# Kernel optimization log

Measured on AMD Instinct MI355X. Metric: run time of the kernel, lower is better.

## Reference

```python
import jax, jax.numpy as jnp
import numpy as np

B, C, H, W = 8, 256, 64, 64
CK = 64  # C // k with k=4


def setup_inputs() -> dict:
    key = jax.random.key(0)
    ks = jax.random.split(key, 5)
    s = 1.0 / np.sqrt(C)
    return {
        "x": jax.random.normal(ks[0], (B, C, H, W), dtype=jnp.float32),
        "wq": jax.random.normal(ks[1], (CK, C), dtype=jnp.float32) * s,
        "bq": jnp.zeros((CK,), dtype=jnp.float32),
        "wk": jax.random.normal(ks[2], (CK, C), dtype=jnp.float32) * s,
        "bk": jnp.zeros((CK,), dtype=jnp.float32),
        "wv": jax.random.normal(ks[3], (C, C), dtype=jnp.float32) * s,
        "bv": jnp.zeros((C,), dtype=jnp.float32),
        "wg": jax.random.normal(ks[4], (C, C), dtype=jnp.float32) * s,
        "bg": jnp.zeros((C,), dtype=jnp.float32),
    }


def reference(x, wq, bq, wk, bk, wv, bv, wg, bg):
    b, c, h, w = x.shape
    n = h * w
    xf = x.reshape(b, c, n)  # [B, C, N]
    # 1x1 convs are channel-wise matmuls
    q = jnp.einsum('oc,bcn->bon', wq, xf) + bq[None, :, None]  # [B, Ck, N]
    k = jnp.einsum('oc,bcn->bon', wk, xf) + bk[None, :, None]  # [B, Ck, N]
    v = jnp.einsum('oc,bcn->bon', wv, xf) + bv[None, :, None]  # [B, C, N]
    # energy[b,i,j] = q[b,:,i] . k[b,:,j]
    energy = jnp.einsum('bci,bcj->bij', q, k)  # [B, N, N]
    energy = jax.nn.elu(energy) / n
    out = jnp.einsum('bcn,bnj->bcj', v, energy).reshape(b, c, h, w)
    out = jnp.einsum('oc,bchw->bohw', wg, out) + bg[None, :, None, None]
    return out
```

## Files before the change

kernel.cpp:

```cpp
#include <hip/hip_runtime.h>
#include <math.h>

#define BATCH 8
#define CH    256
#define NPIX  4096
#define CKDIM 64

typedef __attribute__((ext_vector_type(8))) short short8;
typedef __attribute__((ext_vector_type(4))) float f32x4;

#define MFMA16x16(a, b, c) __builtin_amdgcn_mfma_f32_16x16x32_bf16((a), (b), (c), 0, 0, 0)

__device__ __forceinline__ unsigned short f2bf(float f) {
    union { float f; unsigned int u; } v; v.f = f;
    unsigned int u = v.u;
    u += 0x7fffu + ((u >> 16) & 1u);
    return (unsigned short)(u >> 16);
}

__global__ void prep_kernel(const float* __restrict__ wq, const float* __restrict__ bq,
                            const float* __restrict__ wk, const float* __restrict__ bk,
                            const float* __restrict__ wv, const float* __restrict__ bv,
                            const float* __restrict__ wg,
                            unsigned short* __restrict__ W_frag, float* __restrict__ bias_all) {
    int o = blockIdx.x;
    int c = threadIdx.x;

    float val;
    if (o < 64) {
        val = wq[o * CH + c];
        if (c == 0) bias_all[o] = bq[o];
    } else if (o < 128) {
        int oo = o - 64;
        val = wk[oo * CH + c];
        if (c == 0) bias_all[o] = bk[oo];
    } else {
        __shared__ float wgr[CH];
        int oo = o - 128;
        wgr[c] = wg[oo * CH + c];
        __syncthreads();
        float a0 = 0.f, a1 = 0.f, a2 = 0.f, a3 = 0.f;
#pragma unroll 4
        for (int m = 0; m < CH; m += 4) {
            a0 += wgr[m + 0] * wv[(m + 0) * CH + c];
            a1 += wgr[m + 1] * wv[(m + 1) * CH + c];
            a2 += wgr[m + 2] * wv[(m + 2) * CH + c];
            a3 += wgr[m + 3] * wv[(m + 3) * CH + c];
        }
        val = (a0 + a1) + (a2 + a3);
        if (c == 0) {
            float b = 0.f;
            for (int m = 0; m < CH; ++m) b += wgr[m] * bv[m];
            bias_all[o] = b;
        }
    }

    int og = o >> 6, w = (o >> 4) & 3, col = o & 15;
    int kc = c >> 5, quad = (c >> 3) & 3, e = c & 7;
    size_t idx = ((size_t)(((og * 4 + w) * 8 + kc) * 64 + quad * 16 + col)) * 8 + e;
    W_frag[idx] = f2bf(val);
}

__global__ __launch_bounds__(256, 3)
void qkvf_mfma(const float* __restrict__ x,
               const unsigned short* __restrict__ W_frag,
               const float* __restrict__ bias_all,
               unsigned short* __restrict__ qk, unsigned short* __restrict__ vp) {
    __shared__ float Tl[64][65];
    __shared__ __align__(16) unsigned short Xl[64][264];

    int n0   = blockIdx.x * 64;
    int b    = blockIdx.y;
    int tid  = threadIdx.x;
    int lane = tid & 63;
    int w    = tid >> 6;
    int col  = lane & 15;
    int quad = lane >> 4;

    for (int c0 = 0; c0 < CH; c0 += 64) {
        if (c0) __syncthreads();
#pragma unroll
        for (int r = 0; r < 4; ++r) {
            int f  = r * 256 + tid;
            int c  = f >> 4;
            int n4 = f & 15;
            float4 v = *(const float4*)(x + ((size_t)b * CH + c0 + c) * NPIX + n0 + n4 * 4);
            Tl[n4 * 4 + 0][c] = v.x;
            Tl[n4 * 4 + 1][c] = v.y;
            Tl[n4 * 4 + 2][c] = v.z;
            Tl[n4 * 4 + 3][c] = v.w;
        }
        __syncthreads();
#pragma unroll
        for (int r = 0; r < 2; ++r) {
            int f    = r * 256 + tid;
            int nrow = f >> 3;
            int c8   = f & 7;
            unsigned int pk[4];
#pragma unroll
            for (int p = 0; p < 4; ++p) {
                unsigned int lo = f2bf(Tl[nrow][c8 * 8 + p * 2 + 0]);
                unsigned int hi = f2bf(Tl[nrow][c8 * 8 + p * 2 + 1]);
                pk[p] = lo | (hi << 16);
            }
            *(uint4*)&Xl[nrow][c0 + c8 * 8] = *(uint4*)pk;
        }
    }
    __syncthreads();

#pragma unroll
    for (int og = 0; og < 6; ++og) {
        int o0 = og * 64;
        const unsigned short* Af = W_frag + ((size_t)(og * 32 + w * 8) << 9);

        f32x4 acc[4];
#pragma unroll
        for (int t = 0; t < 4; ++t) acc[t] = (f32x4){0.f, 0.f, 0.f, 0.f};

#pragma unroll
        for (int kc = 0; kc < 8; ++kc) {
            short8 a = *(const short8*)(Af + ((kc << 6) + lane) * 8);
#pragma unroll
            for (int nt = 0; nt < 4; ++nt) {
                short8 bb = *(const short8*)&Xl[nt * 16 + col][kc * 32 + quad * 8];
                acc[nt] = MFMA16x16(a, bb, acc[nt]);
            }
        }

        float4 bias = *(const float4*)(bias_all + o0 + w * 16 + quad * 4);
        float bs[4] = {bias.x, bias.y, bias.z, bias.w};

        if (og < 2) {
#pragma unroll
            for (int nt = 0; nt < 4; ++nt) {
                int n = n0 + nt * 16 + col;
                unsigned int pk[2];
#pragma unroll
                for (int p = 0; p < 2; ++p) {
                    unsigned int lo = f2bf(acc[nt][p * 2 + 0] + bs[p * 2 + 0]);
                    unsigned int hi = f2bf(acc[nt][p * 2 + 1] + bs[p * 2 + 1]);
                    pk[p] = lo | (hi << 16);
                }
                *(uint2*)(qk + ((size_t)b * NPIX + n) * 128 + o0 + w * 16 + quad * 4) = *(uint2*)pk;
            }
        } else {
#pragma unroll
            for (int nt = 0; nt < 4; ++nt) {
                int n = n0 + nt * 16 + col;
#pragma unroll
                for (int r = 0; r < 4; ++r) {
                    int oo = o0 - 128 + w * 16 + quad * 4 + r;
                    vp[((size_t)b * CH + oo) * NPIX + n] = f2bf(acc[nt][r] + bs[r]);
                }
            }
        }
    }
}

#define LPK 72
__global__ __launch_bounds__(512, 4)
void attn_v11(const unsigned short* __restrict__ qk,
              const unsigned short* __restrict__ vp,
              const float* __restrict__ bg, float* __restrict__ out) {
    __shared__ __align__(16) unsigned short Qt[2][64][LPK];
    __shared__ __align__(16) unsigned short St[2][64][LPK];

    int lin  = blockIdx.y * gridDim.x + blockIdx.x;
    int b    = lin & 7;
    int j0   = (lin >> 3) * 64;
    int tid  = threadIdx.x;
    int lane = tid & 63;
    int w    = tid >> 6;
    int col  = lane & 15;
    int quad = lane >> 4;

    int tjA = w & 3;
    int tiP = (w >> 2) * 2;

    short8 bK[2];
#pragma unroll
    for (int ks = 0; ks < 2; ++ks)
        bK[ks] = *(const short8*)(qk + ((size_t)b * NPIX + j0 + tjA * 16 + col) * 128 + 64 + ks * 32 + quad * 8);

    f32x4 acc[2][4];
#pragma unroll
    for (int ot = 0; ot < 2; ++ot)
#pragma unroll
        for (int tj = 0; tj < 4; ++tj) acc[ot][tj] = (f32x4){0.f, 0.f, 0.f, 0.f};

    int qrow = tid >> 3, q8 = tid & 7;
    const unsigned short* Qsrc = qk + ((size_t)b * NPIX + qrow) * 128 + q8 * 8;
    const unsigned short* Vsrc[2];
#pragma unroll
    for (int ot = 0; ot < 2; ++ot)
        Vsrc[ot] = vp + ((size_t)b * CH + (w * 2 + ot) * 16 + col) * NPIX + quad * 8;

    const float invN = 1.f / (float)NPIX;

    {
        uint4 q0 = *(const uint4*)Qsrc;
        *(uint4*)&Qt[0][qrow][q8 * 8] = q0;
    }
    uint4 qrA = *(const uint4*)(Qsrc + (size_t)64 * 128);
    short8 vb[2][2];
#pragma unroll
    for (int ot = 0; ot < 2; ++ot)
#pragma unroll
        for (int ks = 0; ks < 2; ++ks)
            vb[ot][ks] = *(const short8*)(Vsrc[ot] + ks * 32);

    __syncthreads();

#pragma unroll
    for (int t = 0; t < 2; ++t) {
        int ti = tiP + t;
        short8 a0 = *(const short8*)&Qt[0][ti * 16 + col][quad * 8];
        short8 a1 = *(const short8*)&Qt[0][ti * 16 + col][32 + quad * 8];
        f32x4 s = (f32x4){0.f, 0.f, 0.f, 0.f};
        s = MFMA16x16(a0, bK[0], s);
        s = MFMA16x16(a1, bK[1], s);
        unsigned int pk2[2];
#pragma unroll
        for (int pp = 0; pp < 2; ++pp) {
            float e0 = s[pp * 2 + 0];
            float e1 = s[pp * 2 + 1];
            float g0 = __expf(e0) - 1.f;
            float g1 = __expf(e1) - 1.f;
            e0 = (e0 > 0.f) ? e0 : g0;
            e1 = (e1 > 0.f) ? e1 : g1;
            e0 *= invN;
            e1 *= invN;
            unsigned int rpk;
            asm("v_cvt_pk_bf16_f32 %0, %1, %2" : "=v"(rpk) : "v"(e0), "v"(e1));
            pk2[pp] = rpk;
        }
        *(uint2*)&St[0][tjA * 16 + col][ti * 16 + quad * 4] = *(uint2*)pk2;
    }
    *(uint4*)&Qt[1][qrow][q8 * 8] = qrA;
    qrA = *(const uint4*)(Qsrc + (size_t)(2 * 64) * 128);

    for (int it = 1; it < NPIX / 64; ++it) {
        int pw = it & 1;

        __syncthreads();

        *(uint4*)&Qt[pw ^ 1][qrow][q8 * 8] = qrA;

        {
            size_t iq = (size_t)(((it + 2) * 64) & (NPIX - 1));
            qrA = *(const uint4*)(Qsrc + iq * 128);
        }
        int iv = it * 64;
        short8 vb_n[2][2];
#pragma unroll
        for (int ot = 0; ot < 2; ++ot)
#pragma unroll
            for (int ks = 0; ks < 2; ++ks)
                vb_n[ot][ks] = *(const short8*)(Vsrc[ot] + iv + ks * 32);

#pragma unroll
        for (int ks = 0; ks < 2; ++ks) {
            short8 sb[4];
#pragma unroll
            for (int tj = 0; tj < 4; ++tj)
                sb[tj] = *(const short8*)&St[pw ^ 1][tj * 16 + col][ks * 32 + quad * 8];
            __builtin_amdgcn_s_setprio(1);
#pragma unroll
            for (int ot = 0; ot < 2; ++ot)
#pragma unroll
                for (int tj = 0; tj < 4; ++tj)
                    acc[ot][tj] = MFMA16x16(sb[tj], vb[ot][ks], acc[ot][tj]);
            __builtin_amdgcn_s_setprio(0);
        }

#pragma unroll
        for (int t = 0; t < 2; ++t) {
            int ti = tiP + t;
            short8 a0 = *(const short8*)&Qt[pw][ti * 16 + col][quad * 8];
            short8 a1 = *(const short8*)&Qt[pw][ti * 16 + col][32 + quad * 8];
            f32x4 s = (f32x4){0.f, 0.f, 0.f, 0.f};
            s = MFMA16x16(a0, bK[0], s);
            s = MFMA16x16(a1, bK[1], s);
            unsigned int pk2[2];
#pragma unroll
            for (int pp = 0; pp < 2; ++pp) {
                float e0 = s[pp * 2 + 0];
                float e1 = s[pp * 2 + 1];
                float g0 = __expf(e0) - 1.f;
                float g1 = __expf(e1) - 1.f;
                e0 = (e0 > 0.f) ? e0 : g0;
                e1 = (e1 > 0.f) ? e1 : g1;
                e0 *= invN;
                e1 *= invN;
                unsigned int rpk;
                asm("v_cvt_pk_bf16_f32 %0, %1, %2" : "=v"(rpk) : "v"(e0), "v"(e1));
                pk2[pp] = rpk;
            }
            *(uint2*)&St[pw][tjA * 16 + col][ti * 16 + quad * 4] = *(uint2*)pk2;
        }

#pragma unroll
        for (int ot = 0; ot < 2; ++ot)
#pragma unroll
            for (int ks = 0; ks < 2; ++ks)
                vb[ot][ks] = vb_n[ot][ks];
    }

    __syncthreads();
#pragma unroll
    for (int ks = 0; ks < 2; ++ks) {
        short8 sb[4];
#pragma unroll
        for (int tj = 0; tj < 4; ++tj)
            sb[tj] = *(const short8*)&St[1][tj * 16 + col][ks * 32 + quad * 8];
#pragma unroll
        for (int ot = 0; ot < 2; ++ot)
#pragma unroll
            for (int tj = 0; tj < 4; ++tj)
                acc[ot][tj] = MFMA16x16(sb[tj], vb[ot][ks], acc[ot][tj]);
    }

#pragma unroll
    for (int ot = 0; ot < 2; ++ot) {
        int o = (w * 2 + ot) * 16 + col;
        float bgv = bg[o];
#pragma unroll
        for (int tj = 0; tj < 4; ++tj) {
            int j = j0 + tj * 16 + quad * 4;
            float4 st;
            st.x = acc[ot][tj][0] + bgv;
            st.y = acc[ot][tj][1] + bgv;
            st.z = acc[ot][tj][2] + bgv;
            st.w = acc[ot][tj][3] + bgv;
            *(float4*)&out[((size_t)b * CH + o) * NPIX + j] = st;
        }
    }
}

extern "C" void kernel_launch(void* const* d_in, const int* in_sizes, int n_in,
                              void* d_out, int out_size, void* d_ws, size_t ws_size,
                              hipStream_t stream) {
    const float* x  = (const float*)d_in[0];
    const float* wq = (const float*)d_in[1];
    const float* bq = (const float*)d_in[2];
    const float* wk = (const float*)d_in[3];
    const float* bk = (const float*)d_in[4];
    const float* wv = (const float*)d_in[5];
    const float* bv = (const float*)d_in[6];
    const float* wg = (const float*)d_in[7];
    const float* bg = (const float*)d_in[8];
    float* out = (float*)d_out;

    unsigned short* W_frag = (unsigned short*)d_ws;
    float* bias_all = (float*)(W_frag + 384 * 256);
    unsigned short* qk = (unsigned short*)(bias_all + 384);
    unsigned short* vp = qk + (size_t)BATCH * NPIX * 128;

    prep_kernel<<<dim3(384), dim3(256), 0, stream>>>(wq, bq, wk, bk, wv, bv, wg, W_frag, bias_all);
    qkvf_mfma<<<dim3(NPIX / 64, BATCH), dim3(256), 0, stream>>>(x, W_frag, bias_all, qk, vp);
    attn_v11<<<dim3(NPIX / 64, BATCH), dim3(512), 0, stream>>>(qk, vp, bg, out);
}
```

Measured before the change: 244.3 us.

## Load Q fragments directly into registers and fold 1/N scaling into V

Removes the shared-memory Q staging buffer in the attention kernel; each wave now prefetches its Q MFMA fragments straight from global memory one tile ahead. The 1/N normalization moves from the per-element ELU path into the V projection epilogue. This cuts LDS traffic and footprint and saves multiplies in the hot loop, at the cost of redundant, less coalesced global Q loads across waves that share rows.

Result: slower. 370.6 us (+51.7%).

```diff
diff --git a/kernel.cpp b/kernel.cpp
--- a/kernel.cpp
+++ b/kernel.cpp
@@ -150,7 +150,7 @@
 #pragma unroll
                 for (int r = 0; r < 4; ++r) {
                     int oo = o0 - 128 + w * 16 + quad * 4 + r;
-                    vp[((size_t)b * CH + oo) * NPIX + n] = f2bf(acc[nt][r] + bs[r]);
+                    vp[((size_t)b * CH + oo) * NPIX + n] = f2bf((acc[nt][r] + bs[r]) * (1.0f / 4096.0f));
                 }
             }
         }
@@ -159,10 +159,9 @@
 
 #define LPK 72
 __global__ __launch_bounds__(512, 4)
-void attn_v11(const unsigned short* __restrict__ qk,
+void attn_v14(const unsigned short* __restrict__ qk,
               const unsigned short* __restrict__ vp,
               const float* __restrict__ bg, float* __restrict__ out) {
-    __shared__ __align__(16) unsigned short Qt[2][64][LPK];
     __shared__ __align__(16) unsigned short St[2][64][LPK];
 
     int lin  = blockIdx.y * gridDim.x + blockIdx.x;
@@ -188,20 +187,22 @@
 #pragma unroll
         for (int tj = 0; tj < 4; ++tj) acc[ot][tj] = (f32x4){0.f, 0.f, 0.f, 0.f};
 
-    int qrow = tid >> 3, q8 = tid & 7;
-    const unsigned short* Qsrc = qk + ((size_t)b * NPIX + qrow) * 128 + q8 * 8;
+    const unsigned short* Qf[2];
+#pragma unroll
+    for (int t = 0; t < 2; ++t)
+        Qf[t] = qk + ((size_t)b * NPIX + (tiP + t) * 16 + col) * 128 + quad * 8;
+
     const unsigned short* Vsrc[2];
 #pragma unroll
     for (int ot = 0; ot < 2; ++ot)
         Vsrc[ot] = vp + ((size_t)b * CH + (w * 2 + ot) * 16 + col) * NPIX + quad * 8;
 
-    const float invN = 1.f / (float)NPIX;
-
-    {
-        uint4 q0 = *(const uint4*)Qsrc;
-        *(uint4*)&Qt[0][qrow][q8 * 8] = q0;
-    }
-    uint4 qrA = *(const uint4*)(Qsrc + (size_t)64 * 128);
+    short8 qaA[2][2];
+#pragma unroll
+    for (int t = 0; t < 2; ++t)
+#pragma unroll
+        for (int c = 0; c < 2; ++c)
+            qaA[t][c] = *(const short8*)(Qf[t] + c * 32);
     short8 vb[2][2];
 #pragma unroll
     for (int ot = 0; ot < 2; ++ot)
@@ -209,16 +210,12 @@
         for (int ks = 0; ks < 2; ++ks)
             vb[ot][ks] = *(const short8*)(Vsrc[ot] + ks * 32);
 
-    __syncthreads();
-
 #pragma unroll
     for (int t = 0; t < 2; ++t) {
         int ti = tiP + t;
-        short8 a0 = *(const short8*)&Qt[0][ti * 16 + col][quad * 8];
-        short8 a1 = *(const short8*)&Qt[0][ti * 16 + col][32 + quad * 8];
         f32x4 s = (f32x4){0.f, 0.f, 0.f, 0.f};
-        s = MFMA16x16(a0, bK[0], s);
-        s = MFMA16x16(a1, bK[1], s);
+        s = MFMA16x16(qaA[t][0], bK[0], s);
+        s = MFMA16x16(qaA[t][1], bK[1], s);
         unsigned int pk2[2];
 #pragma unroll
         for (int pp = 0; pp < 2; ++pp) {
@@ -228,28 +225,30 @@
             float g1 = __expf(e1) - 1.f;
             e0 = (e0 > 0.f) ? e0 : g0;
             e1 = (e1 > 0.f) ? e1 : g1;
-            e0 *= invN;
-            e1 *= invN;
             unsigned int rpk;
             asm("v_cvt_pk_bf16_f32 %0, %1, %2" : "=v"(rpk) : "v"(e0), "v"(e1));
             pk2[pp] = rpk;
         }
         *(uint2*)&St[0][tjA * 16 + col][ti * 16 + quad * 4] = *(uint2*)pk2;
     }
-    *(uint4*)&Qt[1][qrow][q8 * 8] = qrA;
-    qrA = *(const uint4*)(Qsrc + (size_t)(2 * 64) * 128);
+#pragma unroll
+    for (int t = 0; t < 2; ++t)
+#pragma unroll
+        for (int c = 0; c < 2; ++c)
+            qaA[t][c] = *(const short8*)(Qf[t] + (size_t)64 * 128 + c * 32);
 
     for (int it = 1; it < NPIX / 64; ++it) {
         int pw = it & 1;
 
         __syncthreads();
 
-        *(uint4*)&Qt[pw ^ 1][qrow][q8 * 8] = qrA;
-
-        {
-            size_t iq = (size_t)(((it + 2) * 64) & (NPIX - 1));
-            qrA = *(const uint4*)(Qsrc + iq * 128);
-        }
+        size_t iq = (size_t)(((it + 1) * 64) & (NPIX - 1)) * 128;
+        short8 qa_f[2][2];
+#pragma unroll
+        for (int t = 0; t < 2; ++t)
+#pragma unroll
+            for (int c = 0; c < 2; ++c)
+                qa_f[t][c] = *(const short8*)(Qf[t] + iq + c * 32);
         int iv = it * 64;
         short8 vb_n[2][2];
 #pragma unroll
@@ -276,11 +275,9 @@
 #pragma unroll
         for (int t = 0; t < 2; ++t) {
             int ti = tiP + t;
-            short8 a0 = *(const short8*)&Qt[pw][ti * 16 + col][quad * 8];
-            short8 a1 = *(const short8*)&Qt[pw][ti * 16 + col][32 + quad * 8];
             f32x4 s = (f32x4){0.f, 0.f, 0.f, 0.f};
-            s = MFMA16x16(a0, bK[0], s);
-            s = MFMA16x16(a1, bK[1], s);
+            s = MFMA16x16(qaA[t][0], bK[0], s);
+            s = MFMA16x16(qaA[t][1], bK[1], s);
             unsigned int pk2[2];
 #pragma unroll
             for (int pp = 0; pp < 2; ++pp) {
@@ -290,8 +287,6 @@
                 float g1 = __expf(e1) - 1.f;
                 e0 = (e0 > 0.f) ? e0 : g0;
                 e1 = (e1 > 0.f) ? e1 : g1;
-                e0 *= invN;
-                e1 *= invN;
                 unsigned int rpk;
                 asm("v_cvt_pk_bf16_f32 %0, %1, %2" : "=v"(rpk) : "v"(e0), "v"(e1));
                 pk2[pp] = rpk;
@@ -299,6 +294,11 @@
             *(uint2*)&St[pw][tjA * 16 + col][ti * 16 + quad * 4] = *(uint2*)pk2;
         }
 
+#pragma unroll
+        for (int t = 0; t < 2; ++t)
+#pragma unroll
+            for (int c = 0; c < 2; ++c)
+                qaA[t][c] = qa_f[t][c];
 #pragma unroll
         for (int ot = 0; ot < 2; ++ot)
 #pragma unroll
@@ -358,5 +358,5 @@
 
     prep_kernel<<<dim3(384), dim3(256), 0, stream>>>(wq, bq, wk, bk, wv, bv, wg, W_frag, bias_all);
     qkvf_mfma<<<dim3(NPIX / 64, BATCH), dim3(256), 0, stream>>>(x, W_frag, bias_all, qk, vp);
-    attn_v11<<<dim3(NPIX / 64, BATCH), dim3(512), 0, stream>>>(qk, vp, bg, out);
-}
+    attn_v14<<<dim3(NPIX / 64, BATCH), dim3(512), 0, stream>>>(qk, vp, bg, out);
+}
```
